# Optimization experiments

Measured on AMD Instinct MI355X. Metric: run time of the kernel, lower is better.

Reference implementation:

```python
import jax, jax.numpy as jnp
import numpy as np

NUM_HEADS = 8
MASK_RATE = 0.5


def setup_inputs() -> dict:
    key = jax.random.key(0)
    ks = jax.random.split(key, 6)
    B, N, C = 8, 1024, 256
    TABLE = 10
    att_embedding = jax.random.normal(ks[0], (B, N, C), dtype=jnp.float32)
    relation_position = jax.random.randint(ks[1], (B, N, N), 0, TABLE, dtype=jnp.int32)
    rel_len = jax.random.randint(ks[2], (B,), 0, 20, dtype=jnp.int32)
    W_qkv = jax.random.normal(ks[3], (C, 3 * C), dtype=jnp.float32) * (1.0 / np.sqrt(C))
    W_proj = jax.random.normal(ks[4], (C, C), dtype=jnp.float32) * (1.0 / np.sqrt(C))
    b_proj = jnp.zeros((C,), dtype=jnp.float32)
    bias_table = jax.random.normal(ks[5], (TABLE, NUM_HEADS), dtype=jnp.float32) * 0.02
    return {
        "att_embedding": att_embedding,
        "relation_position": relation_position,
        "rel_len": rel_len,
        "W_qkv": W_qkv,
        "W_proj": W_proj,
        "b_proj": b_proj,
        "bias_table": bias_table,
    }


def reference(att_embedding, relation_position, rel_len, W_qkv, W_proj, b_proj, bias_table):
    B, N, C = att_embedding.shape
    H = NUM_HEADS
    hd = C // H
    scale = hd ** -0.5

    # QKV projection (no bias): [B,N,3C] -> q,k,v each [B,H,N,hd]
    qkv = (att_embedding @ W_qkv).reshape(B, N, 3, H, hd)
    qkv = jnp.transpose(qkv, (2, 0, 3, 1, 4))
    q, k, v = qkv[0], qkv[1], qkv[2]

    # Attention scores [B,H,N,N]
    attn = jnp.einsum("bhnd,bhmd->bhnm", q, k) * scale

    # Relative position bias: gather [B,N,N,H] -> [B,H,N,N]
    pos_bias = jnp.transpose(bias_table[relation_position], (0, 3, 1, 2))

    # Mask bias: table row t gets -100 iff t > mask_len (mask_len+1 .. TABLE-1);
    # identical across heads -> compute as [B,1,N,N] instead of materializing [B,H,N,N].
    mask_len = (rel_len.astype(jnp.float32) * MASK_RATE).astype(jnp.int32)
    mask_bias = jnp.where(relation_position > mask_len[:, None, None], -100.0, 0.0)[:, None]

    attn = jax.nn.softmax(attn + pos_bias + mask_bias, axis=-1)

    # Weighted values -> [B,N,C] -> output projection
    x = jnp.einsum("bhnm,bhmd->bnhd", attn, v).reshape(B, N, C)
    x = x @ W_proj + b_proj
    return x
```

## Files before the change

kernel.cpp:

```cpp
#include <hip/hip_runtime.h>
#include <hip/hip_bf16.h>

typedef __bf16 bf16;
typedef __bf16 bf16x2 __attribute__((ext_vector_type(2)));
typedef __bf16 bf16x8 __attribute__((ext_vector_type(8)));
typedef float f32x4 __attribute__((ext_vector_type(4)));
typedef int i32x4 __attribute__((ext_vector_type(4)));

#define B_ 8
#define N_ 1024
#define C_ 256
#define H_ 8
#define C3_ 768
#define SCALE 0.17677669529663689f
#define FMAX 16.0f


__global__ __launch_bounds__(256) void prep(
    const float* __restrict__ Wqkv, const float* __restrict__ Wproj,
    bf16* __restrict__ Wq_tiled, bf16* __restrict__ Wp_tiled)
{
  int bb = blockIdx.x;
  int o = bb * 256 + threadIdx.x;
  if (bb < 768) {
    int kk = o & 31;
    int idx = o >> 5;
    int nr = idx & 63;
    int qq = idx >> 6;
    int nt = qq % 12, kt = qq / 12;
    int n = nt * 64 + nr, k = kt * 32 + kk;
    Wq_tiled[o] = (bf16)Wqkv[k * C3_ + n];
  } else {
    int p = o - 768 * 256;
    int kk = p & 31;
    int n = (p >> 5) & 255;
    int kt = p >> 13;
    int k = kt * 32 + kk;
    Wp_tiled[p] = (bf16)Wproj[k * C_ + n];
  }
}

__global__ __launch_bounds__(256) void gemm_qkv(
    const float* __restrict__ A, const bf16* __restrict__ Wq_tiled,
    bf16* __restrict__ q, bf16* __restrict__ kT, bf16* __restrict__ vT)
{
  __shared__ bf16 As[64][40];
  __shared__ bf16 Bts[64][40];
  __shared__ bf16 Vls[64][72];

  int tid = threadIdx.x;
  int wave = tid >> 6, lane = tid & 63, quad = lane >> 4, l16 = lane & 15;
  int m0 = blockIdx.x * 64, n0 = blockIdx.y * 64;
  int msub = (wave & 1) * 32, nsub = (wave >> 1) * 32;

  f32x4 acc[2][2] = {};

  int arow = tid >> 2, akc = (tid & 3) * 8;
  const float* aptr = A + (long)(m0 + arow) * C_ + akc;
  const bf16* bptr = Wq_tiled + ((long)(blockIdx.y * 64 + (tid >> 2)) * 32 + (tid & 3) * 8);

  float4 a0 = *reinterpret_cast<const float4*>(aptr);
  float4 a1 = *reinterpret_cast<const float4*>(aptr + 4);
  i32x4 bv = *reinterpret_cast<const i32x4*>(bptr);

  for (int k0 = 0; k0 < C_; k0 += 32) {
    __syncthreads();
    bf16 at[8] = {(bf16)a0.x, (bf16)a0.y, (bf16)a0.z, (bf16)a0.w,
                  (bf16)a1.x, (bf16)a1.y, (bf16)a1.z, (bf16)a1.w};
    *reinterpret_cast<bf16x8*>(&As[arow][akc]) = *reinterpret_cast<bf16x8*>(at);
    *reinterpret_cast<i32x4*>(&Bts[tid >> 2][(tid & 3) * 8]) = bv;
    __syncthreads();

    int kn = k0 + 32;
    if (kn < C_) {
      a0 = *reinterpret_cast<const float4*>(aptr + kn);
      a1 = *reinterpret_cast<const float4*>(aptr + kn + 4);
      bv = *reinterpret_cast<const i32x4*>(bptr + (long)(kn >> 5) * (12 * 64 * 32));
    }

    bf16x8 af0 = *reinterpret_cast<const bf16x8*>(&As[msub + l16][quad * 8]);
    bf16x8 af1 = *reinterpret_cast<const bf16x8*>(&As[msub + 16 + l16][quad * 8]);
    bf16x8 bfr0 = *reinterpret_cast<const bf16x8*>(&Bts[nsub + l16][quad * 8]);
    bf16x8 bfr1 = *reinterpret_cast<const bf16x8*>(&Bts[nsub + 16 + l16][quad * 8]);
    acc[0][0] = __builtin_amdgcn_mfma_f32_16x16x32_bf16(af0, bfr0, acc[0][0], 0, 0, 0);
    acc[0][1] = __builtin_amdgcn_mfma_f32_16x16x32_bf16(af0, bfr1, acc[0][1], 0, 0, 0);
    acc[1][0] = __builtin_amdgcn_mfma_f32_16x16x32_bf16(af1, bfr0, acc[1][0], 0, 0, 0);
    acc[1][1] = __builtin_amdgcn_mfma_f32_16x16x32_bf16(af1, bfr1, acc[1][1], 0, 0, 0);
  }

  if (n0 < 512) {
#pragma unroll
    for (int mi = 0; mi < 2; ++mi)
#pragma unroll
      for (int ni = 0; ni < 2; ++ni)
#pragma unroll
        for (int r = 0; r < 4; ++r) {
          int row = m0 + msub + mi * 16 + quad * 4 + r;
          int col = n0 + nsub + ni * 16 + l16;
          float v = acc[mi][ni][r];
          if (col < 256) {
            q[(long)row * 256 + col] = (bf16)v;
          } else {
            int b = row >> 10, n = row & 1023;
            int c = col - 256, h = c >> 5, d = c & 31;
            kT[(((long)(b * H_ + h)) * N_ + n) * 32 + d] = (bf16)v;
          }
        }
  } else {
    __syncthreads();
#pragma unroll
    for (int mi = 0; mi < 2; ++mi)
#pragma unroll
      for (int ni = 0; ni < 2; ++ni)
#pragma unroll
        for (int r = 0; r < 4; ++r) {
          int cc = nsub + ni * 16 + l16;
          int nn = msub + mi * 16 + quad * 4 + r;
          int np = (nn & 32) | (2 * (nn & 15)) | ((nn >> 4) & 1);
          Vls[cc][np] = (bf16)acc[mi][ni][r];
        }
    __syncthreads();
    int cc = tid >> 2, nn8 = (tid & 3) * 16;
    int b = m0 >> 10;
    long base = ((long)(b * C_ + (n0 - 512) + cc)) * N_ + (m0 & 1023) + nn8;
    *reinterpret_cast<i32x4*>(vT + base) =
        *reinterpret_cast<const i32x4*>(&Vls[cc][nn8]);
    *reinterpret_cast<i32x4*>(vT + base + 8) =
        *reinterpret_cast<const i32x4*>(&Vls[cc][nn8 + 8]);
  }
}

__global__ __launch_bounds__(512) void flash_attn(
    const bf16* __restrict__ q, const bf16* __restrict__ kT,
    const bf16* __restrict__ vT, const int* __restrict__ rel,
    const int* __restrict__ rel_len, const float* __restrict__ btab,
    float* __restrict__ att)
{
  __shared__ bf16 Vs[256][40];
  __shared__ unsigned RelsP[4][33];
  __shared__ bf16 Pls[H_][16 * 40];
  __shared__ float btl[H_][16];

  int tid = threadIdx.x;
  int h = tid >> 6, lane = tid & 63, quad = lane >> 4, l16 = lane & 15;
  int b = blockIdx.y, i0 = blockIdx.x * 16;
  long bN = (long)b * N_;

  int mask_len = (int)((float)rel_len[b] * 0.5f);
  if (tid < 80) {
    int t = tid >> 3, hh = tid & 7;
    btl[hh][t] = btab[t * H_ + hh] + (t > mask_len ? -100.f : 0.f);
  }

  bf16x8 qf = *reinterpret_cast<const bf16x8*>(
      q + (bN + i0 + l16) * 256 + h * 32 + quad * 8);

  const bf16* kbase = kT + ((long)(b * H_ + h)) * N_ * 32 + quad * 8;
  int vrow = tid >> 1, voff = (tid & 1) * 16;
  const bf16* vgp = vT + ((long)b * C_ + vrow) * N_ + voff;
  int rg = tid >> 5, rcol = tid & 31;
  const int* rgp = rel + (bN + i0 + rg * 4) * N_ + rcol;

  bf16x8 kf0 = *reinterpret_cast<const bf16x8*>(kbase + (long)l16 * 32);
  bf16x8 kf1 = *reinterpret_cast<const bf16x8*>(kbase + (long)(16 + l16) * 32);
  bf16x8 vr0 = *reinterpret_cast<const bf16x8*>(vgp);
  bf16x8 vr1 = *reinterpret_cast<const bf16x8*>(vgp + 8);
  int rr0 = 0, rr1 = 0, rr2 = 0, rr3 = 0;
  if (tid < 128) {
    rr0 = rgp[0]; rr1 = rgp[N_]; rr2 = rgp[2 * N_]; rr3 = rgp[3 * N_];
  }

  f32x4 oacc[2] = {};
  float l_part[4] = {0.f, 0.f, 0.f, 0.f};

  for (int j0 = 0; j0 < N_; j0 += 32) {
    __syncthreads();
    *reinterpret_cast<bf16x8*>(&Vs[vrow][voff]) = vr0;
    *reinterpret_cast<bf16x8*>(&Vs[vrow][voff + 8]) = vr1;
    if (tid < 128)
      RelsP[rg][rcol] = (unsigned)rr0 | ((unsigned)rr1 << 8) |
                        ((unsigned)rr2 << 16) | ((unsigned)rr3 << 24);
    __syncthreads();

    int jn = j0 + 32; jn = (jn < N_) ? jn : 0;
    bf16x8 kn0 = *reinterpret_cast<const bf16x8*>(kbase + (long)(jn + l16) * 32);
    bf16x8 kn1 = *reinterpret_cast<const bf16x8*>(kbase + (long)(jn + 16 + l16) * 32);
    vr0 = *reinterpret_cast<const bf16x8*>(vgp + jn);
    vr1 = *reinterpret_cast<const bf16x8*>(vgp + jn + 8);
    if (tid < 128) {
      rr0 = rgp[jn]; rr1 = rgp[N_ + jn]; rr2 = rgp[2 * N_ + jn]; rr3 = rgp[3 * N_ + jn];
    }

    f32x4 z = {};
    f32x4 s0 = __builtin_amdgcn_mfma_f32_16x16x32_bf16(qf, kf0, z, 0, 0, 0);
    f32x4 s1 = __builtin_amdgcn_mfma_f32_16x16x32_bf16(qf, kf1, z, 0, 0, 0);
    kf0 = kn0; kf1 = kn1;

    unsigned w0 = RelsP[quad][l16];
    unsigned w1 = RelsP[quad][16 + l16];
#pragma unroll
    for (int r = 0; r < 4; ++r) {
      int il = quad * 4 + r;
      int rv0 = (w0 >> (8 * r)) & 255;
      int rv1 = (w1 >> (8 * r)) & 255;
      float p0 = __expf(s0[r] * SCALE + btl[h][rv0] - FMAX);
      float p1 = __expf(s1[r] * SCALE + btl[h][rv1] - FMAX);
      l_part[r] += p0 + p1;
      bf16x2 pp = {(bf16)p0, (bf16)p1};
      *reinterpret_cast<bf16x2*>(&Pls[h][il * 40 + l16 * 2]) = pp;
    }
    asm volatile("s_waitcnt lgkmcnt(0)" ::: "memory");
    bf16x8 pf = *reinterpret_cast<const bf16x8*>(&Pls[h][l16 * 40 + quad * 8]);
    bf16x8 vf0 = *reinterpret_cast<const bf16x8*>(&Vs[h * 32 + l16][quad * 8]);
    bf16x8 vf1 = *reinterpret_cast<const bf16x8*>(&Vs[h * 32 + 16 + l16][quad * 8]);
    oacc[0] = __builtin_amdgcn_mfma_f32_16x16x32_bf16(pf, vf0, oacc[0], 0, 0, 0);
    oacc[1] = __builtin_amdgcn_mfma_f32_16x16x32_bf16(pf, vf1, oacc[1], 0, 0, 0);
  }

#pragma unroll
  for (int r = 0; r < 4; ++r) {
    float l = l_part[r];
#pragma unroll
    for (int m = 1; m < 16; m <<= 1) l += __shfl_xor(l, m);
    float inv = 1.f / l;
    long rowoff = (bN + i0 + quad * 4 + r) * C_ + h * 32;
    att[rowoff + l16] = oacc[0][r] * inv;
    att[rowoff + 16 + l16] = oacc[1][r] * inv;
  }
}

__global__ __launch_bounds__(256) void gemm_proj(
    const float* __restrict__ A, const bf16* __restrict__ Wp_tiled,
    const float* __restrict__ bias, float* __restrict__ Cm)
{
  __shared__ bf16 As[16][264];
  __shared__ bf16 Bts[256][40];

  int tid = threadIdx.x;
  int wave = tid >> 6, lane = tid & 63, quad = lane >> 4, l16 = lane & 15;
  int m0 = blockIdx.x * 16;

  {
    int row = tid >> 4, c0 = (tid & 15) * 16;
#pragma unroll
    for (int j8 = 0; j8 < 2; ++j8) {
      float4 v0 = *reinterpret_cast<const float4*>(A + (long)(m0 + row) * C_ + c0 + j8 * 8);
      float4 v1 = *reinterpret_cast<const float4*>(A + (long)(m0 + row) * C_ + c0 + j8 * 8 + 4);
      bf16 at[8] = {(bf16)v0.x, (bf16)v0.y, (bf16)v0.z, (bf16)v0.w,
                    (bf16)v1.x, (bf16)v1.y, (bf16)v1.z, (bf16)v1.w};
      *reinterpret_cast<bf16x8*>(&As[row][c0 + j8 * 8]) = *reinterpret_cast<bf16x8*>(at);
    }
  }

  f32x4 acc[4] = {};
  const bf16* wp = Wp_tiled + (long)tid * 32;

  i32x4 bv0 = *reinterpret_cast<const i32x4*>(wp);
  i32x4 bv1 = *reinterpret_cast<const i32x4*>(wp + 8);
  i32x4 bv2 = *reinterpret_cast<const i32x4*>(wp + 16);
  i32x4 bv3 = *reinterpret_cast<const i32x4*>(wp + 24);

  for (int k0 = 0; k0 < C_; k0 += 32) {
    __syncthreads();
    *reinterpret_cast<i32x4*>(&Bts[tid][0]) = bv0;
    *reinterpret_cast<i32x4*>(&Bts[tid][8]) = bv1;
    *reinterpret_cast<i32x4*>(&Bts[tid][16]) = bv2;
    *reinterpret_cast<i32x4*>(&Bts[tid][24]) = bv3;
    __syncthreads();

    int kn = k0 + 32;
    if (kn < C_) {
      long off = (long)(kn >> 5) * 8192;
      bv0 = *reinterpret_cast<const i32x4*>(wp + off);
      bv1 = *reinterpret_cast<const i32x4*>(wp + off + 8);
      bv2 = *reinterpret_cast<const i32x4*>(wp + off + 16);
      bv3 = *reinterpret_cast<const i32x4*>(wp + off + 24);
    }

    bf16x8 af = *reinterpret_cast<const bf16x8*>(&As[l16][k0 + quad * 8]);
#pragma unroll
    for (int ni = 0; ni < 4; ++ni) {
      bf16x8 bfr = *reinterpret_cast<const bf16x8*>(
          &Bts[wave * 64 + ni * 16 + l16][quad * 8]);
      acc[ni] = __builtin_amdgcn_mfma_f32_16x16x32_bf16(af, bfr, acc[ni], 0, 0, 0);
    }
  }

#pragma unroll
  for (int ni = 0; ni < 4; ++ni)
#pragma unroll
    for (int r = 0; r < 4; ++r) {
      int row = m0 + quad * 4 + r;
      int col = wave * 64 + ni * 16 + l16;
      Cm[(long)row * C_ + col] = acc[ni][r] + bias[col];
    }
}

extern "C" void kernel_launch(void* const* d_in, const int* in_sizes, int n_in,
                              void* d_out, int out_size, void* d_ws, size_t ws_size,
                              hipStream_t stream) {
  const float* X     = (const float*)d_in[0];
  const int*   rel   = (const int*)d_in[1];
  const int*   rlen  = (const int*)d_in[2];
  const float* Wqkv  = (const float*)d_in[3];
  const float* Wproj = (const float*)d_in[4];
  const float* bproj = (const float*)d_in[5];
  const float* btab  = (const float*)d_in[6];
  float* out = (float*)d_out;

  char* ws = (char*)d_ws;
  bf16* Wq_tiled = (bf16*)ws;
  bf16* Wp_tiled = (bf16*)(ws + 393216);
  bf16* q  = (bf16*)(ws + 524288);
  bf16* kT = (bf16*)(ws + 524288 + 4194304);
  bf16* vT = (bf16*)(ws + 524288 + 2 * 4194304);

  prep<<<dim3(1024), 256, 0, stream>>>(Wqkv, Wproj, Wq_tiled, Wp_tiled);
  gemm_qkv<<<dim3(8192 / 64, C3_ / 64), 256, 0, stream>>>(X, Wq_tiled, q, kT, vT);
  flash_attn<<<dim3(N_ / 16, B_), 512, 0, stream>>>(q, kT, vT, rel, rlen, btab, out);
  gemm_proj<<<dim3(8192 / 16), 256, 0, stream>>>(out, Wp_tiled, bproj, out);
}
```

Measured before the change: 143.1 us.

## Fuse output projection into attention, enlarge QKV GEMM tiles, prescale Q

The output projection GEMM is folded into the flash-attention kernel: each block writes its normalized attention tile to shared memory as bf16 and multiplies it by the tiled W_proj with MFMA. This removes a kernel launch and the fp32 round trip of the attention output through global memory. The QKV GEMM moves from 64x64 to 128x128 tiles with 4x4 MFMA accumulators per wave for more operand reuse, at the cost of fewer blocks and higher register pressure. The softmax scale is applied to Q in the GEMM epilogue and the exponent offset is folded into the bias table, which removes per-element multiplies in the attention loop.

New measurement: 140.1 us. -2.1%, faster.

```diff
diff --git a/kernel.cpp b/kernel.cpp
--- a/kernel.cpp
+++ b/kernel.cpp
@@ -44,89 +44,118 @@
     const float* __restrict__ A, const bf16* __restrict__ Wq_tiled,
     bf16* __restrict__ q, bf16* __restrict__ kT, bf16* __restrict__ vT)
 {
-  __shared__ bf16 As[64][40];
-  __shared__ bf16 Bts[64][40];
-  __shared__ bf16 Vls[64][72];
+  __shared__ bf16 As[128][40];
+  __shared__ bf16 Bts[128][40];
+  __shared__ bf16 Vls[64][136];
 
   int tid = threadIdx.x;
   int wave = tid >> 6, lane = tid & 63, quad = lane >> 4, l16 = lane & 15;
-  int m0 = blockIdx.x * 64, n0 = blockIdx.y * 64;
-  int msub = (wave & 1) * 32, nsub = (wave >> 1) * 32;
-
-  f32x4 acc[2][2] = {};
-
-  int arow = tid >> 2, akc = (tid & 3) * 8;
+  int m0 = blockIdx.x * 128, n0 = blockIdx.y * 128;
+  int msub = (wave & 1) * 64, nsub = (wave >> 1) * 64;
+
+  f32x4 acc[4][4] = {};
+
+  int arow = tid >> 1, akc = (tid & 1) * 16;
   const float* aptr = A + (long)(m0 + arow) * C_ + akc;
-  const bf16* bptr = Wq_tiled + ((long)(blockIdx.y * 64 + (tid >> 2)) * 32 + (tid & 3) * 8);
+  int bn = tid >> 1, bkc = (tid & 1) * 16;
+  const bf16* bptr = Wq_tiled +
+      ((long)(blockIdx.y * 2 + (bn >> 6)) * 2048 + (bn & 63) * 32 + bkc);
 
   float4 a0 = *reinterpret_cast<const float4*>(aptr);
   float4 a1 = *reinterpret_cast<const float4*>(aptr + 4);
-  i32x4 bv = *reinterpret_cast<const i32x4*>(bptr);
-
-  for (int k0 = 0; k0 < C_; k0 += 32) {
+  float4 a2 = *reinterpret_cast<const float4*>(aptr + 8);
+  float4 a3 = *reinterpret_cast<const float4*>(aptr + 12);
+  i32x4 bv0 = *reinterpret_cast<const i32x4*>(bptr);
+  i32x4 bv1 = *reinterpret_cast<const i32x4*>(bptr + 8);
+
+  for (int kt = 0; kt < 8; ++kt) {
     __syncthreads();
-    bf16 at[8] = {(bf16)a0.x, (bf16)a0.y, (bf16)a0.z, (bf16)a0.w,
-                  (bf16)a1.x, (bf16)a1.y, (bf16)a1.z, (bf16)a1.w};
-    *reinterpret_cast<bf16x8*>(&As[arow][akc]) = *reinterpret_cast<bf16x8*>(at);
-    *reinterpret_cast<i32x4*>(&Bts[tid >> 2][(tid & 3) * 8]) = bv;
+    {
+      bf16 at[16] = {(bf16)a0.x, (bf16)a0.y, (bf16)a0.z, (bf16)a0.w,
+                     (bf16)a1.x, (bf16)a1.y, (bf16)a1.z, (bf16)a1.w,
+                     (bf16)a2.x, (bf16)a2.y, (bf16)a2.z, (bf16)a2.w,
+                     (bf16)a3.x, (bf16)a3.y, (bf16)a3.z, (bf16)a3.w};
+      *reinterpret_cast<bf16x8*>(&As[arow][akc]) = *reinterpret_cast<bf16x8*>(at);
+      *reinterpret_cast<bf16x8*>(&As[arow][akc + 8]) = *reinterpret_cast<bf16x8*>(at + 8);
+      *reinterpret_cast<i32x4*>(&Bts[bn][bkc]) = bv0;
+      *reinterpret_cast<i32x4*>(&Bts[bn][bkc + 8]) = bv1;
+    }
     __syncthreads();
 
-    int kn = k0 + 32;
-    if (kn < C_) {
+    if (kt < 7) {
+      int kn = (kt + 1) * 32;
       a0 = *reinterpret_cast<const float4*>(aptr + kn);
       a1 = *reinterpret_cast<const float4*>(aptr + kn + 4);
-      bv = *reinterpret_cast<const i32x4*>(bptr + (long)(kn >> 5) * (12 * 64 * 32));
-    }
-
-    bf16x8 af0 = *reinterpret_cast<const bf16x8*>(&As[msub + l16][quad * 8]);
-    bf16x8 af1 = *reinterpret_cast<const bf16x8*>(&As[msub + 16 + l16][quad * 8]);
-    bf16x8 bfr0 = *reinterpret_cast<const bf16x8*>(&Bts[nsub + l16][quad * 8]);
-    bf16x8 bfr1 = *reinterpret_cast<const bf16x8*>(&Bts[nsub + 16 + l16][quad * 8]);
-    acc[0][0] = __builtin_amdgcn_mfma_f32_16x16x32_bf16(af0, bfr0, acc[0][0], 0, 0, 0);
-    acc[0][1] = __builtin_amdgcn_mfma_f32_16x16x32_bf16(af0, bfr1, acc[0][1], 0, 0, 0);
-    acc[1][0] = __builtin_amdgcn_mfma_f32_16x16x32_bf16(af1, bfr0, acc[1][0], 0, 0, 0);
-    acc[1][1] = __builtin_amdgcn_mfma_f32_16x16x32_bf16(af1, bfr1, acc[1][1], 0, 0, 0);
-  }
-
-  if (n0 < 512) {
-#pragma unroll
-    for (int mi = 0; mi < 2; ++mi)
-#pragma unroll
-      for (int ni = 0; ni < 2; ++ni)
+      a2 = *reinterpret_cast<const float4*>(aptr + kn + 8);
+      a3 = *reinterpret_cast<const float4*>(aptr + kn + 12);
+      bv0 = *reinterpret_cast<const i32x4*>(bptr + (long)(kt + 1) * 24576);
+      bv1 = *reinterpret_cast<const i32x4*>(bptr + (long)(kt + 1) * 24576 + 8);
+    }
+
+    bf16x8 af[4], bfr[4];
+#pragma unroll
+    for (int mi = 0; mi < 4; ++mi)
+      af[mi] = *reinterpret_cast<const bf16x8*>(&As[msub + mi * 16 + l16][quad * 8]);
+#pragma unroll
+    for (int ni = 0; ni < 4; ++ni)
+      bfr[ni] = *reinterpret_cast<const bf16x8*>(&Bts[nsub + ni * 16 + l16][quad * 8]);
+#pragma unroll
+    for (int mi = 0; mi < 4; ++mi)
+#pragma unroll
+      for (int ni = 0; ni < 4; ++ni)
+        acc[mi][ni] = __builtin_amdgcn_mfma_f32_16x16x32_bf16(af[mi], bfr[ni], acc[mi][ni], 0, 0, 0);
+  }
+
+  if (n0 < 256) {
+#pragma unroll
+    for (int mi = 0; mi < 4; ++mi)
+#pragma unroll
+      for (int ni = 0; ni < 4; ++ni)
 #pragma unroll
         for (int r = 0; r < 4; ++r) {
           int row = m0 + msub + mi * 16 + quad * 4 + r;
           int col = n0 + nsub + ni * 16 + l16;
-          float v = acc[mi][ni][r];
-          if (col < 256) {
-            q[(long)row * 256 + col] = (bf16)v;
-          } else {
-            int b = row >> 10, n = row & 1023;
-            int c = col - 256, h = c >> 5, d = c & 31;
-            kT[(((long)(b * H_ + h)) * N_ + n) * 32 + d] = (bf16)v;
-          }
+          q[(long)row * 256 + col] = (bf16)(acc[mi][ni][r] * SCALE);
+        }
+  } else if (n0 < 512) {
+#pragma unroll
+    for (int mi = 0; mi < 4; ++mi)
+#pragma unroll
+      for (int ni = 0; ni < 4; ++ni)
+#pragma unroll
+        for (int r = 0; r < 4; ++r) {
+          int row = m0 + msub + mi * 16 + quad * 4 + r;
+          int c = n0 + nsub + ni * 16 + l16 - 256;
+          int b = row >> 10, n = row & 1023;
+          int h = c >> 5, d = c & 31;
+          kT[(((long)(b * H_ + h)) * N_ + n) * 32 + d] = (bf16)acc[mi][ni][r];
         }
   } else {
-    __syncthreads();
-#pragma unroll
-    for (int mi = 0; mi < 2; ++mi)
-#pragma unroll
-      for (int ni = 0; ni < 2; ++ni)
-#pragma unroll
-        for (int r = 0; r < 4; ++r) {
-          int cc = nsub + ni * 16 + l16;
-          int nn = msub + mi * 16 + quad * 4 + r;
-          int np = (nn & 32) | (2 * (nn & 15)) | ((nn >> 4) & 1);
-          Vls[cc][np] = (bf16)acc[mi][ni][r];
-        }
-    __syncthreads();
-    int cc = tid >> 2, nn8 = (tid & 3) * 16;
     int b = m0 >> 10;
-    long base = ((long)(b * C_ + (n0 - 512) + cc)) * N_ + (m0 & 1023) + nn8;
-    *reinterpret_cast<i32x4*>(vT + base) =
-        *reinterpret_cast<const i32x4*>(&Vls[cc][nn8]);
-    *reinterpret_cast<i32x4*>(vT + base + 8) =
-        *reinterpret_cast<const i32x4*>(&Vls[cc][nn8 + 8]);
+#pragma unroll
+    for (int ch = 0; ch < 2; ++ch) {
+      __syncthreads();
+      if ((nsub >> 6) == ch) {
+#pragma unroll
+        for (int mi = 0; mi < 4; ++mi)
+#pragma unroll
+          for (int ni = 0; ni < 4; ++ni)
+#pragma unroll
+            for (int r = 0; r < 4; ++r) {
+              int cc = ni * 16 + l16;
+              int nn = msub + mi * 16 + quad * 4 + r;
+              int np = (nn & 96) | (2 * (nn & 15)) | ((nn >> 4) & 1);
+              Vls[cc][np] = (bf16)acc[mi][ni][r];
+            }
+      }
+      __syncthreads();
+      int cc = tid >> 2, nseg = (tid & 3) * 32;
+      long base = ((long)(b * C_ + (n0 - 512) + ch * 64 + cc)) * N_ + (m0 & 1023) + nseg;
+#pragma unroll
+      for (int j = 0; j < 4; ++j)
+        *reinterpret_cast<i32x4*>(vT + base + j * 8) =
+            *reinterpret_cast<const i32x4*>(&Vls[cc][nseg + j * 8]);
+    }
   }
 }
 
@@ -134,12 +163,14 @@
     const bf16* __restrict__ q, const bf16* __restrict__ kT,
     const bf16* __restrict__ vT, const int* __restrict__ rel,
     const int* __restrict__ rel_len, const float* __restrict__ btab,
-    float* __restrict__ att)
+    const bf16* __restrict__ Wp_tiled, const float* __restrict__ bias,
+    float* __restrict__ out)
 {
   __shared__ bf16 Vs[256][40];
   __shared__ unsigned RelsP[4][33];
   __shared__ bf16 Pls[H_][16 * 40];
   __shared__ float btl[H_][16];
+  __shared__ bf16 attL[16][264];
 
   int tid = threadIdx.x;
   int h = tid >> 6, lane = tid & 63, quad = lane >> 4, l16 = lane & 15;
@@ -149,7 +180,7 @@
   int mask_len = (int)((float)rel_len[b] * 0.5f);
   if (tid < 80) {
     int t = tid >> 3, hh = tid & 7;
-    btl[hh][t] = btab[t * H_ + hh] + (t > mask_len ? -100.f : 0.f);
+    btl[hh][t] = btab[t * H_ + hh] + (t > mask_len ? -100.f : 0.f) - FMAX;
   }
 
   bf16x8 qf = *reinterpret_cast<const bf16x8*>(
@@ -158,7 +189,7 @@
   const bf16* kbase = kT + ((long)(b * H_ + h)) * N_ * 32 + quad * 8;
   int vrow = tid >> 1, voff = (tid & 1) * 16;
   const bf16* vgp = vT + ((long)b * C_ + vrow) * N_ + voff;
-  int rg = tid >> 5, rcol = tid & 31;
+  int rg = (tid >> 5) & 3, rcol = tid & 31;
   const int* rgp = rel + (bN + i0 + rg * 4) * N_ + rcol;
 
   bf16x8 kf0 = *reinterpret_cast<const bf16x8*>(kbase + (long)l16 * 32);
@@ -188,7 +219,8 @@
     vr0 = *reinterpret_cast<const bf16x8*>(vgp + jn);
     vr1 = *reinterpret_cast<const bf16x8*>(vgp + jn + 8);
     if (tid < 128) {
-      rr0 = rgp[jn]; rr1 = rgp[N_ + jn]; rr2 = rgp[2 * N_ + jn]; rr3 = rgp[3 * N_ + jn];
+      rr0 = rgp[jn]; rr1 = rgp[N_ + jn];
+      rr2 = rgp[2 * N_ + jn]; rr3 = rgp[3 * N_ + jn];
     }
 
     f32x4 z = {};
@@ -203,8 +235,8 @@
       int il = quad * 4 + r;
       int rv0 = (w0 >> (8 * r)) & 255;
       int rv1 = (w1 >> (8 * r)) & 255;
-      float p0 = __expf(s0[r] * SCALE + btl[h][rv0] - FMAX);
-      float p1 = __expf(s1[r] * SCALE + btl[h][rv1] - FMAX);
+      float p0 = __expf(s0[r] + btl[h][rv0]);
+      float p1 = __expf(s1[r] + btl[h][rv1]);
       l_part[r] += p0 + p1;
       bf16x2 pp = {(bf16)p0, (bf16)p1};
       *reinterpret_cast<bf16x2*>(&Pls[h][il * 40 + l16 * 2]) = pp;
@@ -223,77 +255,29 @@
 #pragma unroll
     for (int m = 1; m < 16; m <<= 1) l += __shfl_xor(l, m);
     float inv = 1.f / l;
+    attL[quad * 4 + r][h * 32 + l16] = (bf16)(oacc[0][r] * inv);
+    attL[quad * 4 + r][h * 32 + 16 + l16] = (bf16)(oacc[1][r] * inv);
+  }
+  __syncthreads();
+
+  f32x4 pacc[2] = {};
+  const bf16* wp = Wp_tiled + ((h * 32 + l16) * 32 + quad * 8);
+#pragma unroll
+  for (int kt = 0; kt < 8; ++kt) {
+    bf16x8 afr = *reinterpret_cast<const bf16x8*>(&attL[l16][kt * 32 + quad * 8]);
+    bf16x8 b0 = *reinterpret_cast<const bf16x8*>(wp + kt * 8192);
+    bf16x8 b1 = *reinterpret_cast<const bf16x8*>(wp + kt * 8192 + 512);
+    pacc[0] = __builtin_amdgcn_mfma_f32_16x16x32_bf16(afr, b0, pacc[0], 0, 0, 0);
+    pacc[1] = __builtin_amdgcn_mfma_f32_16x16x32_bf16(afr, b1, pacc[1], 0, 0, 0);
+  }
+  float bi0 = bias[h * 32 + l16];
+  float bi1 = bias[h * 32 + 16 + l16];
+#pragma unroll
+  for (int r = 0; r < 4; ++r) {
     long rowoff = (bN + i0 + quad * 4 + r) * C_ + h * 32;
-    att[rowoff + l16] = oacc[0][r] * inv;
-    att[rowoff + 16 + l16] = oacc[1][r] * inv;
-  }
-}
-
-__global__ __launch_bounds__(256) void gemm_proj(
-    const float* __restrict__ A, const bf16* __restrict__ Wp_tiled,
-    const float* __restrict__ bias, float* __restrict__ Cm)
-{
-  __shared__ bf16 As[16][264];
-  __shared__ bf16 Bts[256][40];
-
-  int tid = threadIdx.x;
-  int wave = tid >> 6, lane = tid & 63, quad = lane >> 4, l16 = lane & 15;
-  int m0 = blockIdx.x * 16;
-
-  {
-    int row = tid >> 4, c0 = (tid & 15) * 16;
-#pragma unroll
-    for (int j8 = 0; j8 < 2; ++j8) {
-      float4 v0 = *reinterpret_cast<const float4*>(A + (long)(m0 + row) * C_ + c0 + j8 * 8);
-      float4 v1 = *reinterpret_cast<const float4*>(A + (long)(m0 + row) * C_ + c0 + j8 * 8 + 4);
-      bf16 at[8] = {(bf16)v0.x, (bf16)v0.y, (bf16)v0.z, (bf16)v0.w,
-                    (bf16)v1.x, (bf16)v1.y, (bf16)v1.z, (bf16)v1.w};
-      *reinterpret_cast<bf16x8*>(&As[row][c0 + j8 * 8]) = *reinterpret_cast<bf16x8*>(at);
-    }
-  }
-
-  f32x4 acc[4] = {};
-  const bf16* wp = Wp_tiled + (long)tid * 32;
-
-  i32x4 bv0 = *reinterpret_cast<const i32x4*>(wp);
-  i32x4 bv1 = *reinterpret_cast<const i32x4*>(wp + 8);
-  i32x4 bv2 = *reinterpret_cast<const i32x4*>(wp + 16);
-  i32x4 bv3 = *reinterpret_cast<const i32x4*>(wp + 24);
-
-  for (int k0 = 0; k0 < C_; k0 += 32) {
-    __syncthreads();
-    *reinterpret_cast<i32x4*>(&Bts[tid][0]) = bv0;
-    *reinterpret_cast<i32x4*>(&Bts[tid][8]) = bv1;
-    *reinterpret_cast<i32x4*>(&Bts[tid][16]) = bv2;
-    *reinterpret_cast<i32x4*>(&Bts[tid][24]) = bv3;
-    __syncthreads();
-
-    int kn = k0 + 32;
-    if (kn < C_) {
-      long off = (long)(kn >> 5) * 8192;
-      bv0 = *reinterpret_cast<const i32x4*>(wp + off);
-      bv1 = *reinterpret_cast<const i32x4*>(wp + off + 8);
-      bv2 = *reinterpret_cast<const i32x4*>(wp + off + 16);
-      bv3 = *reinterpret_cast<const i32x4*>(wp + off + 24);
-    }
-
-    bf16x8 af = *reinterpret_cast<const bf16x8*>(&As[l16][k0 + quad * 8]);
-#pragma unroll
-    for (int ni = 0; ni < 4; ++ni) {
-      bf16x8 bfr = *reinterpret_cast<const bf16x8*>(
-          &Bts[wave * 64 + ni * 16 + l16][quad * 8]);
-      acc[ni] = __builtin_amdgcn_mfma_f32_16x16x32_bf16(af, bfr, acc[ni], 0, 0, 0);
-    }
-  }
-
-#pragma unroll
-  for (int ni = 0; ni < 4; ++ni)
-#pragma unroll
-    for (int r = 0; r < 4; ++r) {
-      int row = m0 + quad * 4 + r;
-      int col = wave * 64 + ni * 16 + l16;
-      Cm[(long)row * C_ + col] = acc[ni][r] + bias[col];
-    }
+    out[rowoff + l16] = pacc[0][r] + bi0;
+    out[rowoff + 16 + l16] = pacc[1][r] + bi1;
+  }
 }
 
 extern "C" void kernel_launch(void* const* d_in, const int* in_sizes, int n_in,
@@ -316,7 +300,7 @@
   bf16* vT = (bf16*)(ws + 524288 + 2 * 4194304);
 
   prep<<<dim3(1024), 256, 0, stream>>>(Wqkv, Wproj, Wq_tiled, Wp_tiled);
-  gemm_qkv<<<dim3(8192 / 64, C3_ / 64), 256, 0, stream>>>(X, Wq_tiled, q, kT, vT);
-  flash_attn<<<dim3(N_ / 16, B_), 512, 0, stream>>>(q, kT, vT, rel, rlen, btab, out);
-  gemm_proj<<<dim3(8192 / 16), 256, 0, stream>>>(out, Wp_tiled, bproj, out);
+  gemm_qkv<<<dim3(8192 / 128, C3_ / 128), 256, 0, stream>>>(X, Wq_tiled, q, kT, vT);
+  flash_attn<<<dim3(N_ / 16, B_), 512, 0, stream>>>(
+      q, kT, vT, rel, rlen, btab, Wp_tiled, bproj, out);
 }
```
